# Performance work log

Measured on AMD Instinct MI355X. Metric: run time of the kernel, lower is better.

The kernel has to match this reference:

```python
import jax, jax.numpy as jnp
import numpy as np
from jax import lax

GAT_SLOPE = 0.2   # leaky relu slope inside GATv2 attention
MLP_SLOPE = 0.01  # default nn.LeakyReLU slope in the MLP


def setup_inputs() -> dict:
    key = jax.random.key(0)
    ks = iter(jax.random.split(key, 48))
    nm, nd, C, H = 1500, 800, 128, 8
    E, P = 80000, 40000

    def nrm(shape, s=0.1):
        return jax.random.normal(next(ks), shape, jnp.float32) * s

    inp = {
        "mic_feature": nrm((nm, nm), 1.0),
        "dis_feature": nrm((nd, nd), 1.0),
        "edge_index": jax.random.randint(next(ks), (2, E), 0, nm + nd),
        "pos_pairs": jnp.stack([jax.random.randint(next(ks), (P,), 0, nm),
                                 jax.random.randint(next(ks), (P,), 0, nd)], axis=1),
        "neg_pairs": jnp.stack([jax.random.randint(next(ks), (P,), 0, nm),
                                 jax.random.randint(next(ks), (P,), 0, nd)], axis=1),
        "train_model": 1,
        # projection params
        "W_mic": nrm((nm, C)),
        "W_dis": nrm((nd, C)),
        # GATv2Conv params (lin_l, lin_r, att, out bias); concat=True -> out dim H*C
        "gat_Wl": nrm((C, H * C)),
        "gat_bl": jnp.zeros((H * C,), jnp.float32),
        "gat_Wr": nrm((C, H * C)),
        "gat_br": jnp.zeros((H * C,), jnp.float32),
        "gat_att": nrm((H, C)),
        "gat_bias": jnp.zeros((H * C,), jnp.float32),
        # CNN kernels (heads, k) for k in {1,4,16,32}, 6 out channels
        "cw1": nrm((6, 1, H, 1)),  "cb1": jnp.zeros((6,), jnp.float32),
        "cw4": nrm((6, 1, H, 4)),  "cb4": jnp.zeros((6,), jnp.float32),
        "cw16": nrm((6, 1, H, 16)), "cb16": jnp.zeros((6,), jnp.float32),
        "cw32": nrm((6, 1, H, 32)), "cb32": jnp.zeros((6,), jnp.float32),
        # MLP: 2778 -> 1389 -> 694 -> 463 -> 1 (no bias on last)
        "mw1": nrm((2778, 1389), 0.02), "mb1": jnp.zeros((1389,), jnp.float32),
        "mw2": nrm((1389, 694), 0.02),  "mb2": jnp.zeros((694,), jnp.float32),
        "mw3": nrm((694, 463), 0.02),   "mb3": jnp.zeros((463,), jnp.float32),
        "mw4": nrm((463, 1), 0.05),
    }
    return inp


def _lrelu(x, s):
    return jnp.where(x > 0, x, s * x)


def reference(mic_feature, dis_feature, edge_index, pos_pairs, neg_pairs, train_model,
              W_mic, W_dis, gat_Wl, gat_bl, gat_Wr, gat_br, gat_att, gat_bias,
              cw1, cb1, cw4, cb4, cw16, cb16, cw32, cb32,
              mw1, mb1, mw2, mb2, mw3, mb3, mw4):
    H = gat_att.shape[0]
    # project both node types to common dim and stack: [N, C]
    h = jnp.concatenate([mic_feature @ W_mic, dis_feature @ W_dis], axis=0)
    N, C = h.shape
    # GATv2: separate source/target transforms -> [N, H, C]
    xl = (h @ gat_Wl + gat_bl).reshape(N, H, C)
    xr = (h @ gat_Wr + gat_br).reshape(N, H, C)
    # add self loops (PyG default)
    src = jnp.concatenate([edge_index[0], jnp.arange(N)])
    dst = jnp.concatenate([edge_index[1], jnp.arange(N)])
    z = _lrelu(xl[src] + xr[dst], GAT_SLOPE)           # [E, H, C]
    e = jnp.einsum('ehc,hc->eh', z, gat_att)           # [E, H]
    # segment softmax over incoming edges per destination node
    emax = jax.ops.segment_max(e, dst, num_segments=N)
    ex = jnp.exp(e - emax[dst])
    den = jax.ops.segment_sum(ex, dst, num_segments=N)
    alpha = ex / den[dst]                              # [E, H]
    out = jax.ops.segment_sum(alpha[:, :, None] * xl[src], dst, num_segments=N)
    res = out.reshape(N, H * C) + gat_bias             # [N, H*C]
    # multi-kernel CNN over [N, 1, H, C]
    x4 = res.reshape(N, 1, H, C)

    def conv(w, b):
        y = lax.conv_general_dilated(x4, w, (1, 1), 'VALID',
                                     dimension_numbers=('NCHW', 'OIHW', 'NCHW'))
        return jax.nn.relu(y + b[None, :, None, None]).reshape(N, -1)

    cnn_outputs = jnp.concatenate([conv(cw1, cb1), conv(cw4, cb4),
                                   conv(cw16, cb16), conv(cw32, cb32)], axis=1)
    # vectorized positive/negative pair gather-multiply (replaces python loop)
    nm = mic_feature.shape[0]
    emb_m = cnn_outputs[:nm]
    emb_d = cnn_outputs[nm:]
    pairs = jnp.concatenate([pos_pairs, neg_pairs], axis=0)
    feats = emb_m[pairs[:, 0]] * emb_d[pairs[:, 1]]    # [2P, F]
    labels = jnp.concatenate([jnp.ones((pos_pairs.shape[0], 1), jnp.float32),
                              jnp.zeros((neg_pairs.shape[0], 1), jnp.float32)], axis=0)
    # MLP prediction head (dropout identity at eval)
    hh = _lrelu(feats @ mw1 + mb1, MLP_SLOPE)
    hh = _lrelu(hh @ mw2 + mb2, MLP_SLOPE)
    hh = _lrelu(hh @ mw3 + mb3, MLP_SLOPE)
    pred = jax.nn.sigmoid(hh @ mw4)                    # [2P, 1]
    return (pred, labels, cnn_outputs)
```

## Files before the change

### kernel.cpp

```cpp
#include <hip/hip_runtime.h>


typedef unsigned short u16;
typedef __attribute__((ext_vector_type(8))) short bf16x8;
typedef __attribute__((ext_vector_type(4))) float f32x4;

__device__ __forceinline__ float b2f(u16 u) {
  unsigned v = ((unsigned)u) << 16;
  return __builtin_bit_cast(float, v);
}
__device__ __forceinline__ u16 f2b(float f) {
  unsigned x = __builtin_bit_cast(unsigned, f);
  x += 0x7fffu + ((x >> 16) & 1u);
  return (u16)(x >> 16);
}

__device__ __forceinline__ void async_ld16(const u16* g, u16* l) {
  __builtin_amdgcn_global_load_lds(
      (const __attribute__((address_space(1))) void*)g,
      (__attribute__((address_space(3))) void*)l, 16, 0, 0);
}

__device__ __forceinline__ int sniff_bf16(const void* p, int n) {
  const u16* pu = (const u16*)p;
  int ns = n < 128 ? n : 128;
  int sane = 0, nz = 0;
  for (int i = 0; i < ns; i++) {
    u16 v = pu[i];
    if (v) nz++;
    int e = (v >> 7) & 0xFF;
    if (e >= 100 && e <= 140) sane++;
  }
  return (nz == 0) || (sane * 8 >= ns * 7);
}
__device__ __forceinline__ float ld_any(const void* p, size_t i, int isbf) {
  return isbf ? b2f(((const u16*)p)[i]) : ((const float*)p)[i];
}

__global__ void cvt_f(const void* __restrict__ in, float* __restrict__ out,
                      int n) {
  __shared__ int sbf;
  if (threadIdx.x == 0) sbf = sniff_bf16(in, n);
  __syncthreads();
  int tid = blockIdx.x * 256 + threadIdx.x;
  if (tid < n) out[tid] = ld_any(in, tid, sbf);
}
__global__ void cvt_f_t(const void* __restrict__ in, float* __restrict__ out,
                        int K, int N) {
  __shared__ int sbf;
  if (threadIdx.x == 0) sbf = sniff_bf16(in, K * N);
  __syncthreads();
  int tid = blockIdx.x * 256 + threadIdx.x;
  if (tid >= K * N) return;
  int nn = tid / K, k = tid - nn * K;
  out[tid] = ld_any(in, (size_t)k * N + nn, sbf);
}
__global__ void cvt_b(const void* __restrict__ in, u16* __restrict__ out,
                      int n) {
  __shared__ int sbf;
  if (threadIdx.x == 0) sbf = sniff_bf16(in, n);
  __syncthreads();
  int tid = blockIdx.x * 256 + threadIdx.x;
  if (tid < n) out[tid] = f2b(ld_any(in, tid, sbf));
}
__global__ void cvt_b_tt(const void* __restrict__ in, u16* __restrict__ out,
                         int K, int N, int Kpad, int Npad) {
  __shared__ int sbf;
  __shared__ float tile[32][33];
  if (threadIdx.x == 0) sbf = sniff_bf16(in, K * N);
  __syncthreads();
  int k0 = blockIdx.x * 32, n0 = blockIdx.y * 32;
  int tx = threadIdx.x & 31, ty = threadIdx.x >> 5;
#pragma unroll
  for (int i = 0; i < 32; i += 8) {
    int k = k0 + ty + i, n = n0 + tx;
    tile[ty + i][tx] =
        (k < K && n < N) ? ld_any(in, (size_t)k * N + n, sbf) : 0.f;
  }
  __syncthreads();
#pragma unroll
  for (int i = 0; i < 32; i += 8) {
    int n = n0 + ty + i, k = k0 + tx;
    if (n < Npad && k < Kpad) out[(size_t)n * Kpad + k] = f2b(tile[tx][ty + i]);
  }
}

__global__ void k_feats(const u16* __restrict__ emb,
                        const int* __restrict__ posp,
                        const int* __restrict__ negp, int npos, int mbase,
                        int rows, u16* __restrict__ feats) {
  int idx = blockIdx.x * 256 + threadIdx.x;
  int r = idx / 352, c8 = (idx - r * 352) * 8;
  if (r >= rows) return;
  if (c8 >= 2784) {
    bf16x8 z = {0, 0, 0, 0, 0, 0, 0, 0};
    *(bf16x8*)(feats + (size_t)r * 2816 + c8) = z;
    return;
  }
  int g = mbase + r;
  const int* pp = (g < npos) ? (posp + 2 * g) : (negp + 2 * (g - npos));
  bf16x8 x = *(const bf16x8*)(emb + (size_t)pp[0] * 2784 + c8);
  bf16x8 y = *(const bf16x8*)(emb + (size_t)(1500 + pp[1]) * 2784 + c8);
  bf16x8 v;
#pragma unroll
  for (int j = 0; j < 8; j++)
    ((u16*)&v)[j] = f2b(b2f((u16)x[j]) * b2f((u16)y[j]));
  *(bf16x8*)(feats + (size_t)r * 2816 + c8) = v;
}

__global__ __launch_bounds__(512, 2) void mgemm256(
    const u16* __restrict__ A, const u16* __restrict__ BT,
    const u16* __restrict__ bias, u16* __restrict__ C, int M, int N, int Kpad,
    int lda, int ldb, int ldc, float slope) {
  __shared__ u16 lds[65536];
  u16* As = lds;
  u16* Bs = lds + 32768;
  const int t = threadIdx.x;
  const int lane = t & 63, wave = t >> 6;
  const int quad = lane >> 4, l16 = lane & 15;
  const int wm = wave >> 2, wn = wave & 3;
  const int m0 = blockIdx.y * 256, n0 = blockIdx.x * 256;

  const int r0 = t >> 2;
  const int csrc = (t & 3) ^ ((t >> 3) & 3);
  const u16* Ap = A + (size_t)(m0 + r0) * lda + csrc * 8;
  const u16* Bp = BT + (size_t)(n0 + r0) * ldb + csrc * 8;
  const size_t a128 = (size_t)128 * lda, b128 = (size_t)128 * ldb;
  const int dst = wave * 512;

  const int rsw = (quad ^ ((l16 >> 1) & 3)) * 8;
  const int a_base = (wm * 128 + l16) * 32 + rsw;
  const int b_base = (wn * 64 + l16) * 32 + rsw;

  f32x4 zero4 = {0.f, 0.f, 0.f, 0.f};
  f32x4 acc[8][4];
#pragma unroll
  for (int i = 0; i < 8; i++)
#pragma unroll
    for (int j = 0; j < 4; j++) acc[i][j] = zero4;

  const int iters = Kpad >> 7;

  bf16x8 ra0[4], ra1[4], rb0[4], rb1[4];

#define ST_A(slab, kofs)                              \
  {                                                   \
    u16* d_ = As + (slab) * 8192 + dst;               \
    async_ld16(Ap + (kofs), d_);                      \
    async_ld16(Ap + a128 + (kofs), d_ + 4096);        \
  }
#define ST_B(slab, kofs)                              \
  {                                                   \
    u16* d_ = Bs + (slab) * 8192 + dst;               \
    async_ld16(Bp + (kofs), d_);                      \
    async_ld16(Bp + b128 + (kofs), d_ + 4096);        \
  }
#define LDA4(rr, slab, i0)                                                   \
  _Pragma("unroll") for (int i = 0; i < 4; i++) rr[i] =                      \
      *(const bf16x8*)(As + (slab) * 8192 + a_base + ((i0) + i) * 512);
#define LDB4(rr, slab)                                                       \
  _Pragma("unroll") for (int j = 0; j < 4; j++) rr[j] =                      \
      *(const bf16x8*)(Bs + (slab) * 8192 + b_base + j * 512);
#define BAR __builtin_amdgcn_s_barrier();
#define SBAR __builtin_amdgcn_sched_barrier(0);
#define MFMA16(AS, BS, A0)                                                   \
  _Pragma("unroll") for (int i = 0; i < 4; i++)                              \
      _Pragma("unroll") for (int j = 0; j < 4; j++) acc[(A0) + i][j] =       \
          __builtin_amdgcn_mfma_f32_16x16x32_bf16(AS[i], BS[j],              \
                                                  acc[(A0) + i][j], 0, 0, 0);
#define WAIT6 asm volatile("s_waitcnt vmcnt(6)" ::: "memory");

  ST_A(0, 0);  ST_B(0, 0);
  ST_A(1, 32); ST_B(1, 32);
  ST_A(2, 64); ST_B(2, 64);
  asm volatile("s_waitcnt vmcnt(6)" ::: "memory");
  BAR;
  LDA4(ra0, 0, 0); LDB4(rb0, 0);

  for (int it = 0; it < iters - 1; ++it) {
    const size_t tb = (size_t)it * 128;
    BAR; ST_A(3, tb + 96);          LDA4(ra1, 0, 4);               SBAR; MFMA16(ra0, rb0, 0);
    BAR; ST_B(3, tb + 96);  WAIT6;  LDA4(ra0, 1, 0); LDB4(rb1, 1); SBAR; MFMA16(ra1, rb0, 4);
    BAR; ST_A(0, tb + 128);         LDA4(ra1, 1, 4);               SBAR; MFMA16(ra0, rb1, 0);
    BAR; ST_B(0, tb + 128); WAIT6;  LDA4(ra0, 2, 0); LDB4(rb0, 2); SBAR; MFMA16(ra1, rb1, 4);
    BAR; ST_A(1, tb + 160);         LDA4(ra1, 2, 4);               SBAR; MFMA16(ra0, rb0, 0);
    BAR; ST_B(1, tb + 160); WAIT6;  LDA4(ra0, 3, 0); LDB4(rb1, 3); SBAR; MFMA16(ra1, rb0, 4);
    BAR; ST_A(2, tb + 192);         LDA4(ra1, 3, 4);               SBAR; MFMA16(ra0, rb1, 0);
    BAR; ST_B(2, tb + 192); WAIT6;  LDA4(ra0, 0, 0); LDB4(rb0, 0); SBAR; MFMA16(ra1, rb1, 4);
  }

  {
    const size_t tb = (size_t)(iters - 1) * 128;
    BAR; ST_A(3, tb + 96);          LDA4(ra1, 0, 4);               SBAR; MFMA16(ra0, rb0, 0);
    BAR; ST_B(3, tb + 96);
    asm volatile("s_waitcnt vmcnt(8)" ::: "memory");
    LDA4(ra0, 1, 0); LDB4(rb1, 1);                                 SBAR; MFMA16(ra1, rb0, 4);
    BAR;                            LDA4(ra1, 1, 4);               SBAR; MFMA16(ra0, rb1, 0);
    BAR;
    asm volatile("s_waitcnt vmcnt(4)" ::: "memory");
    LDA4(ra0, 2, 0); LDB4(rb0, 2);                                 SBAR; MFMA16(ra1, rb1, 4);
    BAR;                            LDA4(ra1, 2, 4);               SBAR; MFMA16(ra0, rb0, 0);
    BAR;
    asm volatile("s_waitcnt vmcnt(0)" ::: "memory");
    LDA4(ra0, 3, 0); LDB4(rb1, 3);                                 SBAR; MFMA16(ra1, rb0, 4);
    BAR;                            LDA4(ra1, 3, 4);               SBAR; MFMA16(ra0, rb1, 0);
    BAR;                                                           SBAR; MFMA16(ra1, rb1, 4);
  }
#undef ST_A
#undef ST_B
#undef LDA4
#undef LDB4
#undef BAR
#undef SBAR
#undef MFMA16
#undef WAIT6

#pragma unroll
  for (int j = 0; j < 4; j++) {
    int col = n0 + wn * 64 + j * 16 + l16;
    if (col >= ldc) continue;
    float bv = 0.f;
    if (bias != nullptr && col < N) bv = b2f(bias[col]);
#pragma unroll
    for (int i = 0; i < 8; i++) {
#pragma unroll
      for (int r = 0; r < 4; r++) {
        int row = m0 + wm * 128 + i * 16 + quad * 4 + r;
        if (row >= M) continue;
        float v;
        if (col < N) {
          v = acc[i][j][r] + bv;
          v = (v > 0.f) ? v : v * slope;
        } else {
          v = 0.f;
        }
        C[(size_t)row * ldc + col] = f2b(v);
      }
    }
  }
}

__global__ __launch_bounds__(256) void vgemm_f(
    const float* __restrict__ A, const float* __restrict__ BT,
    const float* __restrict__ bias, float* __restrict__ C, int M, int N, int K,
    int lda, int ldb, int ldc) {
  __shared__ float As[16 * 66];
  __shared__ float Bs[64 * 66];
  const int t = threadIdx.x;
  const int m0 = blockIdx.y * 16, n0 = blockIdx.x * 64;
  const int tx = t & 63, ty = t >> 6;
  float acc[4] = {0.f, 0.f, 0.f, 0.f};
  for (int k0 = 0; k0 < K; k0 += 64) {
    for (int idx = t; idx < 16 * 64; idx += 256) {
      int r = idx >> 6, k = idx & 63;
      int m = m0 + r, kk = k0 + k;
      As[r * 66 + k] = (m < M && kk < K) ? A[(size_t)m * lda + kk] : 0.f;
    }
    for (int idx = t; idx < 64 * 64; idx += 256) {
      int nr = idx >> 6, k = idx & 63;
      int nn = n0 + nr, kk = k0 + k;
      Bs[nr * 66 + k] = (nn < N && kk < K) ? BT[(size_t)nn * ldb + kk] : 0.f;
    }
    __syncthreads();
#pragma unroll 8
    for (int k = 0; k < 64; k++) {
      float b = Bs[tx * 66 + k];
#pragma unroll
      for (int q = 0; q < 4; q++) acc[q] += As[(ty * 4 + q) * 66 + k] * b;
    }
    __syncthreads();
  }
  int col = n0 + tx;
  if (col >= N) return;
  float bv = (bias != nullptr) ? bias[col] : 0.f;
#pragma unroll
  for (int q = 0; q < 4; q++) {
    int row = m0 + ty * 4 + q;
    if (row < M) C[(size_t)row * ldc + col] = acc[q] + bv;
  }
}

__global__ __launch_bounds__(256) void vgemm_ks(
    const float* __restrict__ A, const float* __restrict__ BT,
    float* __restrict__ C, int M, int N, int K, int lda, int ldb, int ldc,
    int kchunk) {
  __shared__ float As[16 * 66];
  __shared__ float Bs[64 * 66];
  const int t = threadIdx.x;
  const int m0 = blockIdx.y * 16, n0 = blockIdx.x * 64;
  const int kbeg = blockIdx.z * kchunk;
  int kend = kbeg + kchunk;
  if (kend > K) kend = K;
  const int tx = t & 63, ty = t >> 6;
  float acc[4] = {0.f, 0.f, 0.f, 0.f};
  for (int k0 = kbeg; k0 < kend; k0 += 64) {
    for (int idx = t; idx < 16 * 64; idx += 256) {
      int r = idx >> 6, k = idx & 63;
      int m = m0 + r, kk = k0 + k;
      As[r * 66 + k] = (m < M && kk < kend) ? A[(size_t)m * lda + kk] : 0.f;
    }
    for (int idx = t; idx < 64 * 64; idx += 256) {
      int nr = idx >> 6, k = idx & 63;
      int nn = n0 + nr, kk = k0 + k;
      Bs[nr * 66 + k] = (nn < N && kk < kend) ? BT[(size_t)nn * ldb + kk] : 0.f;
    }
    __syncthreads();
#pragma unroll 8
    for (int k = 0; k < 64; k++) {
      float b = Bs[tx * 66 + k];
#pragma unroll
      for (int q = 0; q < 4; q++) acc[q] += As[(ty * 4 + q) * 66 + k] * b;
    }
    __syncthreads();
  }
  int col = n0 + tx;
  if (col >= N) return;
#pragma unroll
  for (int q = 0; q < 4; q++) {
    int row = m0 + ty * 4 + q;
    if (row < M) atomicAdd(&C[(size_t)row * ldc + col], acc[q]);
  }
}

__global__ void k_zero2(int* __restrict__ a, int* __restrict__ b, int n) {
  int tid = blockIdx.x * 256 + threadIdx.x;
  if (tid < n) { a[tid] = 0; b[tid] = 0; }
}

__global__ void k_zerof(float* __restrict__ a, int n) {
  int tid = blockIdx.x * 256 + threadIdx.x;
  if (tid < n) a[tid] = 0.f;
}

__global__ void k_edge_e(const float* __restrict__ xl,
                         const float* __restrict__ xr,
                         const int* __restrict__ ei,
                         const float* __restrict__ att, float* __restrict__ e,
                         int E, int Etot) {
  __shared__ float attf[1024];
  int t = threadIdx.x;
  for (int i = t; i < 1024; i += 256) attf[i] = att[i];
  __syncthreads();
  int lane = t & 63;
  int eid = blockIdx.x * 4 + (t >> 6);
  if (eid >= Etot) return;
  int src = (eid < E) ? ei[eid] : (eid - E);
  int dst = (eid < E) ? ei[E + eid] : (eid - E);
  const float* pl = xl + (size_t)src * 1024;
  const float* pr = xr + (size_t)dst * 1024;
#pragma unroll
  for (int h = 0; h < 8; h++) {
    float a0 = pl[h * 128 + lane] + pr[h * 128 + lane];
    float a1 = pl[h * 128 + 64 + lane] + pr[h * 128 + 64 + lane];
    a0 = (a0 > 0.f) ? a0 : 0.2f * a0;
    a1 = (a1 > 0.f) ? a1 : 0.2f * a1;
    float p = a0 * attf[h * 128 + lane] + a1 * attf[h * 128 + 64 + lane];
#pragma unroll
    for (int off = 32; off; off >>= 1) p += __shfl_xor(p, off);
    if (lane == 0) e[(size_t)eid * 8 + h] = p;
  }
}

__global__ void k_count(const int* __restrict__ ei, int* __restrict__ cnt,
                        int E, int Etot) {
  int tid = blockIdx.x * 256 + threadIdx.x;
  if (tid >= Etot) return;
  int dst = (tid < E) ? ei[E + tid] : (tid - E);
  atomicAdd(&cnt[dst], 1);
}

__global__ void k_scan(const int* __restrict__ cnt, int* __restrict__ rowstart,
                       int Nn) {
  __shared__ int part[257];
  int t = threadIdx.x;
  int chunk = (Nn + 255) / 256;
  int b = t * chunk;
  int en = b + chunk; if (en > Nn) en = Nn;
  int s = 0;
  for (int i = b; i < en; i++) s += cnt[i];
  part[t] = s;
  __syncthreads();
  if (t == 0) {
    int acc = 0;
    for (int i = 0; i < 256; i++) { int v = part[i]; part[i] = acc; acc += v; }
    part[256] = acc;
  }
  __syncthreads();
  int run = part[t];
  for (int i = b; i < en; i++) { rowstart[i] = run; run += cnt[i]; }
  if (t == 0) rowstart[Nn] = part[256];
}

__global__ void k_scatter(const int* __restrict__ ei,
                          const int* __restrict__ rowstart,
                          int* __restrict__ cur, int* __restrict__ csr, int E,
                          int Etot) {
  int tid = blockIdx.x * 256 + threadIdx.x;
  if (tid >= Etot) return;
  int dst = (tid < E) ? ei[E + tid] : (tid - E);
  int p = atomicAdd(&cur[dst], 1);
  unsigned idx = (unsigned)(rowstart[dst] + p);
  if (idx < (unsigned)Etot) csr[idx] = tid;
}

__global__ void k_softmax(const float* __restrict__ e,
                          const int* __restrict__ csr,
                          const int* __restrict__ rowstart,
                          float* __restrict__ wgt, int Nn, int Etot) {
  int t = threadIdx.x;
  int lane = t & 63;
  int d = blockIdx.x * 4 + (t >> 6);
  if (d >= Nn) return;
  int rs = rowstart[d], re = rowstart[d + 1];
  for (int h = 0; h < 8; h++) {
    float mx = -3.0e38f;
    for (int i = rs + lane; i < re; i += 64) {
      unsigned eid = (unsigned)csr[i];
      if (eid < (unsigned)Etot) mx = fmaxf(mx, e[(size_t)eid * 8 + h]);
    }
#pragma unroll
    for (int off = 32; off; off >>= 1) mx = fmaxf(mx, __shfl_xor(mx, off));
    if (mx < -1.0e37f) mx = 0.f;
    float s = 0.f;
    for (int i = rs + lane; i < re; i += 64) {
      unsigned eid = (unsigned)csr[i];
      if (eid < (unsigned)Etot) s += expf(e[(size_t)eid * 8 + h] - mx);
    }
#pragma unroll
    for (int off = 32; off; off >>= 1) s += __shfl_xor(s, off);
    float inv = (s > 0.f) ? 1.f / s : 0.f;
    for (int i = rs + lane; i < re; i += 64) {
      unsigned eid = (unsigned)csr[i];
      if (eid < (unsigned)Etot)
        wgt[(size_t)eid * 8 + h] = expf(e[(size_t)eid * 8 + h] - mx) * inv;
    }
  }
}

__global__ void k_aggregate(const float* __restrict__ wgt,
                            const float* __restrict__ xl,
                            const int* __restrict__ ei,
                            const int* __restrict__ csr,
                            const int* __restrict__ rowstart,
                            const float* __restrict__ gbias,
                            float* __restrict__ res, int E, int Etot) {
  int d = blockIdx.x;
  int t = threadIdx.x;
  int c = t & 127, hb = t >> 7;
  int rs = rowstart[d], re = rowstart[d + 1];
  float acc[4] = {0.f, 0.f, 0.f, 0.f};
  for (int i = rs; i < re; i++) {
    unsigned eid = (unsigned)csr[i];
    if (eid >= (unsigned)Etot) continue;
    int src = (eid < (unsigned)E) ? ei[eid] : (int)(eid - E);
    const float* px = xl + (size_t)src * 1024 + hb * 512 + c;
    const float* pw = wgt + (size_t)eid * 8 + hb * 4;
#pragma unroll
    for (int q = 0; q < 4; q++) acc[q] += pw[q] * px[q * 128];
  }
#pragma unroll
  for (int q = 0; q < 4; q++) {
    int idx = (hb * 4 + q) * 128 + c;
    res[(size_t)d * 1024 + idx] = acc[q] + gbias[idx];
  }
}

__global__ void k_cnn(const float* __restrict__ res,
                      const float* __restrict__ cw1, const float* __restrict__ cb1,
                      const float* __restrict__ cw4, const float* __restrict__ cb4,
                      const float* __restrict__ cw16, const float* __restrict__ cb16,
                      const float* __restrict__ cw32, const float* __restrict__ cb32,
                      float* __restrict__ outc, u16* __restrict__ emb) {
  __shared__ float xs[1024];
  __shared__ float wc[2544];
  __shared__ float cb[24];
  int t = threadIdx.x, node = blockIdx.x;
  for (int i = t; i < 1024; i += 256) xs[i] = res[(size_t)node * 1024 + i];
  for (int i = t; i < 48; i += 256) wc[i] = cw1[i];
  for (int i = t; i < 192; i += 256) wc[48 + i] = cw4[i];
  for (int i = t; i < 768; i += 256) wc[240 + i] = cw16[i];
  for (int i = t; i < 1536; i += 256) wc[1008 + i] = cw32[i];
  if (t < 6) {
    cb[t] = cb1[t];
    cb[6 + t] = cb4[t];
    cb[12 + t] = cb16[t];
    cb[18 + t] = cb32[t];
  }
  __syncthreads();
  for (int o = t; o < 2778; o += 256) {
    int k, W, base, boff, rr;
    if (o < 768)       { k = 1;  W = 128; base = 0;    boff = 0;  rr = o; }
    else if (o < 1518) { k = 4;  W = 125; base = 48;   boff = 6;  rr = o - 768; }
    else if (o < 2196) { k = 16; W = 113; base = 240;  boff = 12; rr = o - 1518; }
    else               { k = 32; W = 97;  base = 1008; boff = 18; rr = o - 2196; }
    int oc = rr / W, wp = rr - oc * W;
    const float* wgt = &wc[base + oc * 8 * k];
    float v = cb[boff + oc];
    for (int h = 0; h < 8; h++)
      for (int j = 0; j < k; j++) v += xs[h * 128 + wp + j] * wgt[h * k + j];
    v = fmaxf(v, 0.f);
    outc[(size_t)node * 2778 + o] = v;
    emb[(size_t)node * 2784 + o] = f2b(v);
  }
  if (t < 6) emb[(size_t)node * 2784 + 2778 + t] = 0;
}

__global__ void k_gemv_sig(const u16* __restrict__ hh3,
                           const u16* __restrict__ w4, float* __restrict__ pred,
                           int M, int K, int ldk) {
  __shared__ float ws[464];
  int t = threadIdx.x;
  for (int i = t; i < K; i += 256) ws[i] = b2f(w4[i]);
  __syncthreads();
  int lane = t & 63;
  int m = blockIdx.x * 4 + (t >> 6);
  if (m >= M) return;
  const u16* p = hh3 + (size_t)m * ldk;
  float s = 0.f;
  for (int i = lane; i < K; i += 64) s += b2f(p[i]) * ws[i];
#pragma unroll
  for (int off = 32; off; off >>= 1) s += __shfl_xor(s, off);
  if (!(s == s)) s = 0.f;
  s = fminf(fmaxf(s, -30.f), 30.f);
  if (lane == 0) pred[m] = 1.f / (1.f + expf(-s));
}

__global__ void k_labels(float* __restrict__ lab, int P) {
  int tid = blockIdx.x * 256 + threadIdx.x;
  if (tid < 2 * P) lab[tid] = (tid < P) ? 1.f : 0.f;
}

__global__ void k_sentinel(float* __restrict__ pred, int M, float val) {
  int tid = blockIdx.x * 256 + threadIdx.x;
  if (tid < M) pred[tid] = val;
}

extern "C" void kernel_launch(void* const* d_in, const int* in_sizes, int n_in,
                              void* d_out, int out_size, void* d_ws,
                              size_t ws_size, hipStream_t stream) {
  (void)in_sizes; (void)n_in; (void)out_size;
  const int* ei = (const int*)d_in[2];
  const int* posp = (const int*)d_in[3];
  const int* negp = (const int*)d_in[4];

  const int E = 80000, ET = 82300, P = 40000, M = 80000;

  float* outp = (float*)d_out;
  float* outl = outp + 80000;
  float* outc = outp + 160000;

  k_labels<<<(2 * P + 255) / 256, 256, 0, stream>>>(outl, P);

  char* base = (char*)d_ws;
  size_t off = 0;
  auto alloc = [&](size_t bytes) -> void* {
    void* p = base + off;
    off = (off + bytes + 255) & ~(size_t)255;
    return p;
  };
  float* mic_f = (float*)alloc((size_t)1500 * 1500 * 4);
  float* dis_f = (float*)alloc((size_t)800 * 800 * 4);
  float* WmT_f = (float*)alloc((size_t)128 * 1500 * 4);
  float* WdT_f = (float*)alloc((size_t)128 * 800 * 4);
  float* WlT_f = (float*)alloc((size_t)1024 * 128 * 4);
  float* WrT_f = (float*)alloc((size_t)1024 * 128 * 4);
  float* bl_f = (float*)alloc(1024 * 4);
  float* br_f = (float*)alloc(1024 * 4);
  float* att_f = (float*)alloc(1024 * 4);
  float* gbias_f = (float*)alloc(1024 * 4);
  float* cw1_f = (float*)alloc(48 * 4);
  float* cb1_f = (float*)alloc(6 * 4);
  float* cw4_f = (float*)alloc(192 * 4);
  float* cb4_f = (float*)alloc(6 * 4);
  float* cw16_f = (float*)alloc(768 * 4);
  float* cb16_f = (float*)alloc(6 * 4);
  float* cw32_f = (float*)alloc(1536 * 4);
  float* cb32_f = (float*)alloc(6 * 4);
  u16* m1T = (u16*)alloc((size_t)1536 * 2816 * 2);
  u16* m2T = (u16*)alloc((size_t)768 * 1408 * 2);
  u16* m3T = (u16*)alloc((size_t)512 * 768 * 2);
  u16* mb1_b = (u16*)alloc(1389 * 2);
  u16* mb2_b = (u16*)alloc(694 * 2);
  u16* mb3_b = (u16*)alloc(463 * 2);
  u16* mw4_b = (u16*)alloc(463 * 2);
  float* hbuf = (float*)alloc((size_t)2300 * 128 * 4);
  float* xlf = (float*)alloc((size_t)2300 * 1024 * 4);
  float* xrf = (float*)alloc((size_t)2300 * 1024 * 4);
  float* resf = xrf;
  float* ebuf = (float*)alloc((size_t)ET * 8 * 4);
  float* wbuf = (float*)alloc((size_t)ET * 8 * 4);
  u16* emb = (u16*)alloc((size_t)2300 * 2784 * 2);
  int* cnt = (int*)alloc(2300 * 4);
  int* rowst = (int*)alloc(2304 * 4);
  int* cur = (int*)alloc(2300 * 4);
  int* csr = (int*)alloc((size_t)ET * 4);
  size_t fixed_end = off;

  const size_t per_row = (size_t)(2816 + 1408 + 768) * 2;
  size_t avail = (ws_size > fixed_end) ? (ws_size - fixed_end) : 0;
  long long Rll = (long long)(avail / per_row);
  int R = (Rll > M) ? M : (int)Rll;
  R &= ~255;
  if (R > 21760) R = 21760;
  if (fixed_end > ws_size || R < 256) {
    k_sentinel<<<(M + 255) / 256, 256, 0, stream>>>(outp, M, 0.25f);
    return;
  }
  u16* feats = (u16*)(base + fixed_end);
  u16* hh1 = feats + (size_t)R * 2816;
  u16* hh2 = hh1 + (size_t)R * 1408;

  k_zero2<<<(2300 + 255) / 256, 256, 0, stream>>>(cnt, cur, 2300);
  k_zerof<<<(2300 * 128 + 255) / 256, 256, 0, stream>>>(hbuf, 2300 * 128);

  cvt_f<<<(2250000 + 255) / 256, 256, 0, stream>>>(d_in[0], mic_f, 2250000);
  cvt_f<<<(640000 + 255) / 256, 256, 0, stream>>>(d_in[1], dis_f, 640000);
  cvt_f_t<<<(192000 + 255) / 256, 256, 0, stream>>>(d_in[6], WmT_f, 1500, 128);
  cvt_f_t<<<(102400 + 255) / 256, 256, 0, stream>>>(d_in[7], WdT_f, 800, 128);
  cvt_f_t<<<(131072 + 255) / 256, 256, 0, stream>>>(d_in[8], WlT_f, 128, 1024);
  cvt_f<<<4, 256, 0, stream>>>(d_in[9], bl_f, 1024);
  cvt_f_t<<<(131072 + 255) / 256, 256, 0, stream>>>(d_in[10], WrT_f, 128, 1024);
  cvt_f<<<4, 256, 0, stream>>>(d_in[11], br_f, 1024);
  cvt_f<<<4, 256, 0, stream>>>(d_in[12], att_f, 1024);
  cvt_f<<<4, 256, 0, stream>>>(d_in[13], gbias_f, 1024);
  cvt_f<<<1, 256, 0, stream>>>(d_in[14], cw1_f, 48);
  cvt_f<<<1, 256, 0, stream>>>(d_in[15], cb1_f, 6);
  cvt_f<<<1, 256, 0, stream>>>(d_in[16], cw4_f, 192);
  cvt_f<<<1, 256, 0, stream>>>(d_in[17], cb4_f, 6);
  cvt_f<<<3, 256, 0, stream>>>(d_in[18], cw16_f, 768);
  cvt_f<<<1, 256, 0, stream>>>(d_in[19], cb16_f, 6);
  cvt_f<<<6, 256, 0, stream>>>(d_in[20], cw32_f, 1536);
  cvt_f<<<1, 256, 0, stream>>>(d_in[21], cb32_f, 6);
  cvt_b_tt<<<dim3(88, 48), 256, 0, stream>>>(d_in[22], m1T, 2778, 1389, 2816,
                                             1536);
  cvt_b<<<(1389 + 255) / 256, 256, 0, stream>>>(d_in[23], mb1_b, 1389);
  cvt_b_tt<<<dim3(44, 24), 256, 0, stream>>>(d_in[24], m2T, 1389, 694, 1408,
                                             768);
  cvt_b<<<(694 + 255) / 256, 256, 0, stream>>>(d_in[25], mb2_b, 694);
  cvt_b_tt<<<dim3(24, 16), 256, 0, stream>>>(d_in[26], m3T, 694, 463, 768, 512);
  cvt_b<<<(463 + 255) / 256, 256, 0, stream>>>(d_in[27], mb3_b, 463);
  cvt_b<<<(463 + 255) / 256, 256, 0, stream>>>(d_in[28], mw4_b, 463);

  vgemm_ks<<<dim3(2, 94, 8), 256, 0, stream>>>(mic_f, WmT_f, hbuf, 1500, 128,
                                               1500, 1500, 1500, 128, 192);
  vgemm_ks<<<dim3(2, 50, 5), 256, 0, stream>>>(dis_f, WdT_f,
                                               hbuf + (size_t)1500 * 128, 800,
                                               128, 800, 800, 800, 128, 192);
  vgemm_f<<<dim3(16, 144), 256, 0, stream>>>(hbuf, WlT_f, bl_f, xlf, 2300,
                                             1024, 128, 128, 128, 1024);
  vgemm_f<<<dim3(16, 144), 256, 0, stream>>>(hbuf, WrT_f, br_f, xrf, 2300,
                                             1024, 128, 128, 128, 1024);

  k_edge_e<<<(ET + 3) / 4, 256, 0, stream>>>(xlf, xrf, ei, att_f, ebuf, E, ET);
  k_count<<<(ET + 255) / 256, 256, 0, stream>>>(ei, cnt, E, ET);
  k_scan<<<1, 256, 0, stream>>>(cnt, rowst, 2300);
  k_scatter<<<(ET + 255) / 256, 256, 0, stream>>>(ei, rowst, cur, csr, E, ET);
  k_softmax<<<(2300 + 3) / 4, 256, 0, stream>>>(ebuf, csr, rowst, wbuf, 2300, ET);
  k_aggregate<<<2300, 256, 0, stream>>>(wbuf, xlf, ei, csr, rowst, gbias_f,
                                        resf, E, ET);

  k_cnn<<<2300, 256, 0, stream>>>(resf, cw1_f, cb1_f, cw4_f, cb4_f, cw16_f,
                                  cb16_f, cw32_f, cb32_f, outc, emb);

  for (int c0 = 0; c0 < M; c0 += R) {
    int rows = (M - c0 < R) ? (M - c0) : R;
    int gby = (rows + 255) / 256;
    k_feats<<<((size_t)rows * 352 + 255) / 256, 256, 0, stream>>>(
        emb, posp, negp, P, c0, rows, feats);
    mgemm256<<<dim3(6, gby), 512, 0, stream>>>(feats, m1T, mb1_b, hh1, rows,
                                               1389, 2816, 2816, 2816, 1408,
                                               0.01f);
    mgemm256<<<dim3(3, gby), 512, 0, stream>>>(hh1, m2T, mb2_b, hh2, rows, 694,
                                               1408, 1408, 1408, 768, 0.01f);
    mgemm256<<<dim3(2, gby), 512, 0, stream>>>(hh2, m3T, mb3_b, hh1, rows, 463,
                                               768, 768, 768, 480, 0.01f);
    k_gemv_sig<<<(rows + 3) / 4, 256, 0, stream>>>(hh1, mw4_b, outp + c0, rows,
                                                   463, 480);
  }
}
```

Before: 1.993 ms.

## Load GEMM B fragments directly from global into registers, halve LDS

The MLP GEMM kernel no longer stages the B (weight) tile through shared memory. Each wave now loads its B fragments straight from global memory into registers, while A keeps its async LDS pipeline, so LDS use drops from 128KB to 64KB per block. Waits are adjusted to the reduced count of outstanding loads. The hh2 buffer is also aliased onto feats to lower workspace per row, which raises the row chunk R. In exchange, B global loads now sit more directly on the critical path, and B reuse across the 4 row-waves relies on cache instead of LDS.

```diff
diff --git a/kernel.cpp b/kernel.cpp
--- a/kernel.cpp
+++ b/kernel.cpp
@@ -112,9 +112,7 @@
     const u16* __restrict__ A, const u16* __restrict__ BT,
     const u16* __restrict__ bias, u16* __restrict__ C, int M, int N, int Kpad,
     int lda, int ldb, int ldc, float slope) {
-  __shared__ u16 lds[65536];
-  u16* As = lds;
-  u16* Bs = lds + 32768;
+  __shared__ u16 As[32768];
   const int t = threadIdx.x;
   const int lane = t & 63, wave = t >> 6;
   const int quad = lane >> 4, l16 = lane & 15;
@@ -124,13 +122,13 @@
   const int r0 = t >> 2;
   const int csrc = (t & 3) ^ ((t >> 3) & 3);
   const u16* Ap = A + (size_t)(m0 + r0) * lda + csrc * 8;
-  const u16* Bp = BT + (size_t)(n0 + r0) * ldb + csrc * 8;
-  const size_t a128 = (size_t)128 * lda, b128 = (size_t)128 * ldb;
+  const size_t a128 = (size_t)128 * lda;
   const int dst = wave * 512;
 
   const int rsw = (quad ^ ((l16 >> 1) & 3)) * 8;
   const int a_base = (wm * 128 + l16) * 32 + rsw;
-  const int b_base = (wn * 64 + l16) * 32 + rsw;
+
+  const u16* Bw = BT + (size_t)(n0 + wn * 64 + l16) * ldb + quad * 8;
 
   f32x4 zero4 = {0.f, 0.f, 0.f, 0.f};
   f32x4 acc[8][4];
@@ -149,18 +147,12 @@
     async_ld16(Ap + (kofs), d_);                      \
     async_ld16(Ap + a128 + (kofs), d_ + 4096);        \
   }
-#define ST_B(slab, kofs)                              \
-  {                                                   \
-    u16* d_ = Bs + (slab) * 8192 + dst;               \
-    async_ld16(Bp + (kofs), d_);                      \
-    async_ld16(Bp + b128 + (kofs), d_ + 4096);        \
-  }
 #define LDA4(rr, slab, i0)                                                   \
   _Pragma("unroll") for (int i = 0; i < 4; i++) rr[i] =                      \
       *(const bf16x8*)(As + (slab) * 8192 + a_base + ((i0) + i) * 512);
-#define LDB4(rr, slab)                                                       \
+#define GLB4(rr, kofs)                                                       \
   _Pragma("unroll") for (int j = 0; j < 4; j++) rr[j] =                      \
-      *(const bf16x8*)(Bs + (slab) * 8192 + b_base + j * 512);
+      *(const bf16x8*)(Bw + (size_t)(j * 16) * ldb + (kofs));
 #define BAR __builtin_amdgcn_s_barrier();
 #define SBAR __builtin_amdgcn_sched_barrier(0);
 #define MFMA16(AS, BS, A0)                                                   \
@@ -168,52 +160,50 @@
       _Pragma("unroll") for (int j = 0; j < 4; j++) acc[(A0) + i][j] =       \
           __builtin_amdgcn_mfma_f32_16x16x32_bf16(AS[i], BS[j],              \
                                                   acc[(A0) + i][j], 0, 0, 0);
-#define WAIT6 asm volatile("s_waitcnt vmcnt(6)" ::: "memory");
-
-  ST_A(0, 0);  ST_B(0, 0);
-  ST_A(1, 32); ST_B(1, 32);
-  ST_A(2, 64); ST_B(2, 64);
-  asm volatile("s_waitcnt vmcnt(6)" ::: "memory");
+#define WAIT4 asm volatile("s_waitcnt vmcnt(4)" ::: "memory");
+#define WAIT2 asm volatile("s_waitcnt vmcnt(2)" ::: "memory");
+#define WAIT0 asm volatile("s_waitcnt vmcnt(0)" ::: "memory");
+
+  ST_A(0, 0);
+  ST_A(1, 32);
+  ST_A(2, 64);
+  WAIT4;
   BAR;
-  LDA4(ra0, 0, 0); LDB4(rb0, 0);
+  GLB4(rb0, 0);
+  LDA4(ra0, 0, 0);
 
   for (int it = 0; it < iters - 1; ++it) {
     const size_t tb = (size_t)it * 128;
-    BAR; ST_A(3, tb + 96);          LDA4(ra1, 0, 4);               SBAR; MFMA16(ra0, rb0, 0);
-    BAR; ST_B(3, tb + 96);  WAIT6;  LDA4(ra0, 1, 0); LDB4(rb1, 1); SBAR; MFMA16(ra1, rb0, 4);
-    BAR; ST_A(0, tb + 128);         LDA4(ra1, 1, 4);               SBAR; MFMA16(ra0, rb1, 0);
-    BAR; ST_B(0, tb + 128); WAIT6;  LDA4(ra0, 2, 0); LDB4(rb0, 2); SBAR; MFMA16(ra1, rb1, 4);
-    BAR; ST_A(1, tb + 160);         LDA4(ra1, 2, 4);               SBAR; MFMA16(ra0, rb0, 0);
-    BAR; ST_B(1, tb + 160); WAIT6;  LDA4(ra0, 3, 0); LDB4(rb1, 3); SBAR; MFMA16(ra1, rb0, 4);
-    BAR; ST_A(2, tb + 192);         LDA4(ra1, 3, 4);               SBAR; MFMA16(ra0, rb1, 0);
-    BAR; ST_B(2, tb + 192); WAIT6;  LDA4(ra0, 0, 0); LDB4(rb0, 0); SBAR; MFMA16(ra1, rb1, 4);
+    BAR; ST_A(3, tb + 96);                  LDA4(ra1, 0, 4); SBAR; MFMA16(ra0, rb0, 0);
+    BAR; WAIT4; GLB4(rb1, tb + 32);         LDA4(ra0, 1, 0); SBAR; MFMA16(ra1, rb0, 4);
+    BAR; ST_A(0, tb + 128);                 LDA4(ra1, 1, 4); SBAR; MFMA16(ra0, rb1, 0);
+    BAR; WAIT4; GLB4(rb0, tb + 64);         LDA4(ra0, 2, 0); SBAR; MFMA16(ra1, rb1, 4);
+    BAR; ST_A(1, tb + 160);                 LDA4(ra1, 2, 4); SBAR; MFMA16(ra0, rb0, 0);
+    BAR; WAIT4; GLB4(rb1, tb + 96);         LDA4(ra0, 3, 0); SBAR; MFMA16(ra1, rb0, 4);
+    BAR; ST_A(2, tb + 192);                 LDA4(ra1, 3, 4); SBAR; MFMA16(ra0, rb1, 0);
+    BAR; WAIT4; GLB4(rb0, tb + 128);        LDA4(ra0, 0, 0); SBAR; MFMA16(ra1, rb1, 4);
   }
 
   {
     const size_t tb = (size_t)(iters - 1) * 128;
-    BAR; ST_A(3, tb + 96);          LDA4(ra1, 0, 4);               SBAR; MFMA16(ra0, rb0, 0);
-    BAR; ST_B(3, tb + 96);
-    asm volatile("s_waitcnt vmcnt(8)" ::: "memory");
-    LDA4(ra0, 1, 0); LDB4(rb1, 1);                                 SBAR; MFMA16(ra1, rb0, 4);
-    BAR;                            LDA4(ra1, 1, 4);               SBAR; MFMA16(ra0, rb1, 0);
-    BAR;
-    asm volatile("s_waitcnt vmcnt(4)" ::: "memory");
-    LDA4(ra0, 2, 0); LDB4(rb0, 2);                                 SBAR; MFMA16(ra1, rb1, 4);
-    BAR;                            LDA4(ra1, 2, 4);               SBAR; MFMA16(ra0, rb0, 0);
-    BAR;
-    asm volatile("s_waitcnt vmcnt(0)" ::: "memory");
-    LDA4(ra0, 3, 0); LDB4(rb1, 3);                                 SBAR; MFMA16(ra1, rb0, 4);
-    BAR;                            LDA4(ra1, 3, 4);               SBAR; MFMA16(ra0, rb1, 0);
-    BAR;                                                           SBAR; MFMA16(ra1, rb1, 4);
+    BAR; ST_A(3, tb + 96);                  LDA4(ra1, 0, 4); SBAR; MFMA16(ra0, rb0, 0);
+    BAR; WAIT4; GLB4(rb1, tb + 32);         LDA4(ra0, 1, 0); SBAR; MFMA16(ra1, rb0, 4);
+    BAR;                                    LDA4(ra1, 1, 4); SBAR; MFMA16(ra0, rb1, 0);
+    BAR; WAIT2; GLB4(rb0, tb + 64);         LDA4(ra0, 2, 0); SBAR; MFMA16(ra1, rb1, 4);
+    BAR;                                    LDA4(ra1, 2, 4); SBAR; MFMA16(ra0, rb0, 0);
+    BAR; WAIT0; GLB4(rb1, tb + 96);         LDA4(ra0, 3, 0); SBAR; MFMA16(ra1, rb0, 4);
+    BAR;                                    LDA4(ra1, 3, 4); SBAR; MFMA16(ra0, rb1, 0);
+    SBAR; MFMA16(ra1, rb1, 4);
   }
 #undef ST_A
-#undef ST_B
 #undef LDA4
-#undef LDB4
+#undef GLB4
 #undef BAR
 #undef SBAR
 #undef MFMA16
-#undef WAIT6
+#undef WAIT4
+#undef WAIT2
+#undef WAIT0
 
 #pragma unroll
   for (int j = 0; j < 4; j++) {
@@ -596,7 +586,7 @@
   int* csr = (int*)alloc((size_t)ET * 4);
   size_t fixed_end = off;
 
-  const size_t per_row = (size_t)(2816 + 1408 + 768) * 2;
+  const size_t per_row = (size_t)(2816 + 1408) * 2;
   size_t avail = (ws_size > fixed_end) ? (ws_size - fixed_end) : 0;
   long long Rll = (long long)(avail / per_row);
   int R = (Rll > M) ? M : (int)Rll;
@@ -608,7 +598,7 @@
   }
   u16* feats = (u16*)(base + fixed_end);
   u16* hh1 = feats + (size_t)R * 2816;
-  u16* hh2 = hh1 + (size_t)R * 1408;
+  u16* hh2 = feats;
 
   k_zero2<<<(2300 + 255) / 256, 256, 0, stream>>>(cnt, cur, 2300);
   k_zerof<<<(2300 * 128 + 255) / 256, 256, 0, stream>>>(hbuf, 2300 * 128);
```

Result: slower. 2.512 ms (+26.0%).
